# Kernel tuning notes

Hardware: AMD Instinct MI355X
Metric: run time of the kernel (lower is better)

Reference implementation:

```python
import jax, jax.numpy as jnp
import numpy as np

B, C, D = 4096, 1000, 3072


def setup_inputs() -> dict:
    key = jax.random.key(0)
    k1, k2, k3, k4 = jax.random.split(key, 4)
    scale = 1.0
    return {
        "z": jax.random.normal(k1, (B, D), dtype=jnp.float32),
        "sldj": jax.random.normal(k2, (B,), dtype=jnp.float32),
        "labels": jax.random.randint(k3, (B,), 0, C),
        "beta": jnp.ones((), dtype=jnp.float32),
        "means": jax.random.normal(k4, (C, D), dtype=jnp.float32) * scale,
    }


def reference(z, sldj, labels, beta, means):
    # dists[i,j] = -0.5 * ||z_i - mu_j||^2, via a^2 + b^2 - 2ab GEMM trick
    z2 = jnp.sum(z * z, axis=1, keepdims=True)          # [B,1]
    m2 = jnp.sum(means * means, axis=1)[None, :]        # [1,C]
    cross = jnp.einsum('bd,cd->bc', z, means)           # [B,C] GEMM
    dists = -0.5 * (z2 + m2 - 2.0 * cross)              # [B,C]

    log_pz = jax.nn.logsumexp(dists, axis=1)            # [B]
    # cross_entropy(dists, labels) = mean(logsumexp - dists[i, y_i])
    picked = jnp.take_along_axis(dists, labels[:, None], axis=1)[:, 0]
    loss_cls = jnp.mean(log_pz - picked)
    loss_gen = -jnp.mean(log_pz + sldj) / z.shape[1]
    total = loss_gen + beta * loss_cls
    return total, loss_gen, loss_cls
```

## Files before the change

### kernel.cpp

```cpp
#include <hip/hip_runtime.h>
#include <hip/hip_bf16.h>
#include <cstdint>
#include <cstddef>

#define NB 4096
#define NC 1000
#define NCP 1024
#define ND 3072
#define NSL 4
#define KSL (ND / NSL)
#define BM 128
#define BN 128
#define BK 32
#define NT (KSL / BK)
#define ABUF (BM * BK)
#define BBUF (BN * BK)

typedef __attribute__((ext_vector_type(8))) __bf16 bf16x8;
typedef __attribute__((ext_vector_type(4))) float f32x4;
typedef __attribute__((ext_vector_type(4))) unsigned short u16x4;
typedef __attribute__((ext_vector_type(4))) _Float16 f16x4;
typedef unsigned short u16;

__device__ __forceinline__ u16 f2bf_rne(float x) {
    uint32_t u = __float_as_uint(x);
    uint32_t r = (u + 0x7fffu + ((u >> 16) & 1u)) >> 16;
    return (u16)r;
}

__global__ __launch_bounds__(256) void convert_means_kernel(
        const float* __restrict__ means, u16* __restrict__ mb,
        float* __restrict__ m2) {
    const int row = blockIdx.x;
    const int tid = threadIdx.x;
    u16* dst = mb + (size_t)row * ND;
    if (row < NC) {
        const float4* s = (const float4*)(means + (size_t)row * ND);
        float acc = 0.f;
#pragma unroll
        for (int i = 0; i < 3; ++i) {
            const int idx = tid + i * 256;
            float4 v = s[idx];
            acc = fmaf(v.x, v.x, acc);
            acc = fmaf(v.y, v.y, acc);
            acc = fmaf(v.z, v.z, acc);
            acc = fmaf(v.w, v.w, acc);
            u16x4 o;
            o.x = f2bf_rne(v.x); o.y = f2bf_rne(v.y);
            o.z = f2bf_rne(v.z); o.w = f2bf_rne(v.w);
            *(u16x4*)(dst + idx * 4) = o;
        }
#pragma unroll
        for (int off = 32; off > 0; off >>= 1) acc += __shfl_xor(acc, off, 64);
        __shared__ float ssum[4];
        const int wid = tid >> 6, lane = tid & 63;
        if (lane == 0) ssum[wid] = acc;
        __syncthreads();
        if (tid == 0) m2[row] = ssum[0] + ssum[1] + ssum[2] + ssum[3];
    } else {
        u16x4 z4 = (u16x4){0, 0, 0, 0};
#pragma unroll
        for (int i = 0; i < 3; ++i) *(u16x4*)(dst + (tid + i * 256) * 4) = z4;
        if (tid == 0) m2[row] = 1e30f;
    }
}

#define GLOAD_LDS16(gp, lp)                                            \
    __builtin_amdgcn_global_load_lds(                                  \
        (const __attribute__((address_space(1))) void*)(gp),           \
        (__attribute__((address_space(3))) void*)(lp), 16, 0, 0)

__global__ __launch_bounds__(256, 4) void gemm_kernel(
        const float* __restrict__ z, const u16* __restrict__ mb,
        _Float16* __restrict__ crossh, float* __restrict__ z2p) {
    __shared__ u16 As[2 * ABUF];
    __shared__ u16 Bs[2 * BBUF];

    const int tid  = threadIdx.x;
    const int wid  = tid >> 6;
    const int lane = tid & 63;
    const int wr   = wid >> 1;
    const int wc   = wid & 1;
    const int lrow = lane & 15;
    const int kgrp = lane >> 4;

    const int bid = blockIdx.x;
    const int w = (bid & 7) * 128 + (bid >> 3);
    const int bcol8 = w & 7;
    const int brow  = ((w >> 3) & 31) * BM;
    const int ksl   = w >> 8;
    const int bcol  = bcol8 * BN;
    const int kbase = ksl * KSL;
    const bool do_ssq = (bcol8 == 0);

    f32x4 acc[4][4];
#pragma unroll
    for (int m = 0; m < 4; ++m)
#pragma unroll
        for (int n = 0; n < 4; ++n) acc[m][n] = (f32x4){0.f, 0.f, 0.f, 0.f};

    const float* gA[4];
    u16* wAp[4];
#pragma unroll
    for (int g = 0; g < 4; ++g) {
        const int c = g * 256 + tid;
        const int r = c >> 3, q = c & 7;
        const int p = (q >> 1) ^ ((r >> 1) & 3);
        gA[g]  = z + (size_t)(brow + r) * ND + kbase + q * 4;
        wAp[g] = As + r * BK + p * 8 + (q & 1) * 4;
    }
    const u16* gB[2];
    u16* lB[2];
#pragma unroll
    for (int g = 0; g < 2; ++g) {
        const int c = g * 256 + tid;
        const int r = c >> 2, p = c & 3, s = p ^ ((r >> 1) & 3);
        gB[g] = mb + (size_t)(bcol + r) * ND + kbase + s * 8;
        lB[g] = Bs + (g * 256 + wid * 64) * 8;
    }

    float4 areg[4];
    float ssq0 = 0.f, ssq1 = 0.f, ssq2 = 0.f, ssq3 = 0.f;

#define ISSUE(tt, nb_) do {                                              \
        const int ko_ = (tt) * BK;                                       \
        areg[0] = *(const float4*)(gA[0] + ko_);                         \
        areg[1] = *(const float4*)(gA[1] + ko_);                         \
        areg[2] = *(const float4*)(gA[2] + ko_);                         \
        areg[3] = *(const float4*)(gA[3] + ko_);                         \
        GLOAD_LDS16(gB[0] + ko_, lB[0] + (nb_) * BBUF);                  \
        GLOAD_LDS16(gB[1] + ko_, lB[1] + (nb_) * BBUF);                  \
    } while (0)

#define WRITEA(nb_) do {                                                 \
        _Pragma("unroll")                                                \
        for (int g = 0; g < 4; ++g) {                                    \
            u16x4 o;                                                     \
            o.x = f2bf_rne(areg[g].x); o.y = f2bf_rne(areg[g].y);        \
            o.z = f2bf_rne(areg[g].z); o.w = f2bf_rne(areg[g].w);        \
            *(u16x4*)(wAp[g] + (nb_) * ABUF) = o;                        \
        }                                                                \
        if (do_ssq) {                                                    \
            ssq0 = fmaf(areg[0].x, areg[0].x, fmaf(areg[0].y, areg[0].y, \
                   fmaf(areg[0].z, areg[0].z, fmaf(areg[0].w, areg[0].w, ssq0)))); \
            ssq1 = fmaf(areg[1].x, areg[1].x, fmaf(areg[1].y, areg[1].y, \
                   fmaf(areg[1].z, areg[1].z, fmaf(areg[1].w, areg[1].w, ssq1)))); \
            ssq2 = fmaf(areg[2].x, areg[2].x, fmaf(areg[2].y, areg[2].y, \
                   fmaf(areg[2].z, areg[2].z, fmaf(areg[2].w, areg[2].w, ssq2)))); \
            ssq3 = fmaf(areg[3].x, areg[3].x, fmaf(areg[3].y, areg[3].y, \
                   fmaf(areg[3].z, areg[3].z, fmaf(areg[3].w, areg[3].w, ssq3)))); \
        }                                                                \
    } while (0)

#define COMP(tt) do {                                                    \
        const int cb_ = (tt) & 1;                                        \
        const u16* Ac = As + cb_ * ABUF;                                 \
        const u16* Bc = Bs + cb_ * BBUF;                                 \
        const int pk = kgrp ^ ((lrow >> 1) & 3);                         \
        bf16x8 a0 = *(const bf16x8*)&Ac[(wr * 64 +  0 + lrow) * BK + pk * 8]; \
        bf16x8 a1 = *(const bf16x8*)&Ac[(wr * 64 + 16 + lrow) * BK + pk * 8]; \
        bf16x8 a2 = *(const bf16x8*)&Ac[(wr * 64 + 32 + lrow) * BK + pk * 8]; \
        bf16x8 a3 = *(const bf16x8*)&Ac[(wr * 64 + 48 + lrow) * BK + pk * 8]; \
        _Pragma("unroll")                                                \
        for (int n = 0; n < 4; ++n) {                                    \
            bf16x8 bn = *(const bf16x8*)&Bc[(wc * 64 + n * 16 + lrow) * BK + pk * 8]; \
            acc[0][n] = __builtin_amdgcn_mfma_f32_16x16x32_bf16(a0, bn, acc[0][n], 0, 0, 0); \
            acc[1][n] = __builtin_amdgcn_mfma_f32_16x16x32_bf16(a1, bn, acc[1][n], 0, 0, 0); \
            acc[2][n] = __builtin_amdgcn_mfma_f32_16x16x32_bf16(a2, bn, acc[2][n], 0, 0, 0); \
            acc[3][n] = __builtin_amdgcn_mfma_f32_16x16x32_bf16(a3, bn, acc[3][n], 0, 0, 0); \
        }                                                                \
    } while (0)

    ISSUE(0, 0);
    asm volatile("s_waitcnt vmcnt(0)" ::: "memory");
    WRITEA(0);
    asm volatile("s_waitcnt lgkmcnt(0)" ::: "memory");
    __builtin_amdgcn_s_barrier();
    __builtin_amdgcn_sched_barrier(0);

    for (int t = 0; t < NT; ++t) {
        const int nxt = (t + 1) & 1;
        if (t + 1 < NT) ISSUE(t + 1, nxt);
        __builtin_amdgcn_sched_barrier(0);
        COMP(t);
        if (t + 1 < NT) {
            asm volatile("s_waitcnt vmcnt(0)" ::: "memory");
            WRITEA(nxt);
        }
        asm volatile("s_waitcnt lgkmcnt(0)" ::: "memory");
        __builtin_amdgcn_s_barrier();
        __builtin_amdgcn_sched_barrier(0);
    }

#undef ISSUE
#undef WRITEA
#undef COMP

    if (do_ssq) {
        float* sb = (float*)As;
        sb[0 * 256 + tid] = ssq0;
        sb[1 * 256 + tid] = ssq1;
        sb[2 * 256 + tid] = ssq2;
        sb[3 * 256 + tid] = ssq3;
        __syncthreads();
        if (tid < BM) {
            const int g = tid >> 5;
            const int base = (tid * 8) & 255;
            float s = 0.f;
#pragma unroll
            for (int j = 0; j < 8; ++j) s += sb[g * 256 + base + j];
            z2p[(size_t)ksl * NB + brow + tid] = s;
        }
    }

    _Float16* outp = crossh + (size_t)ksl * NB * NCP;
#pragma unroll
    for (int n = 0; n < 4; ++n) {
        const int gcol = bcol + wc * 64 + n * 16 + lrow;
#pragma unroll
        for (int m = 0; m < 4; ++m) {
#pragma unroll
            for (int r = 0; r < 4; ++r) {
                const int grow = brow + wr * 64 + m * 16 + kgrp * 4 + r;
                outp[(size_t)grow * NCP + gcol] = (_Float16)acc[m][n][r];
            }
        }
    }
}

__global__ __launch_bounds__(256) void row_lse_kernel(
        const _Float16* __restrict__ crossh, const float* __restrict__ m2,
        const int* __restrict__ labels, const float* __restrict__ sldj,
        float* __restrict__ outA, float* __restrict__ outB) {
    const int row = blockIdx.x;
    const int tid = threadIdx.x;

    float a0 = 0.f, a1 = 0.f, a2 = 0.f, a3 = 0.f;
#pragma unroll
    for (int s = 0; s < NSL; ++s) {
        f16x4 h = ((const f16x4*)(crossh + ((size_t)s * NB + row) * NCP))[tid];
        a0 += (float)h.x; a1 += (float)h.y; a2 += (float)h.z; a3 += (float)h.w;
    }
    float4 mm = ((const float4*)m2)[tid];
    float4 v;
    v.x = a0 - 0.5f * mm.x;
    v.y = a1 - 0.5f * mm.y;
    v.z = a2 - 0.5f * mm.z;
    v.w = a3 - 0.5f * mm.w;

    float mx = fmaxf(fmaxf(v.x, v.y), fmaxf(v.z, v.w));
#pragma unroll
    for (int off = 32; off > 0; off >>= 1) mx = fmaxf(mx, __shfl_xor(mx, off, 64));
    __shared__ float smax[4], ssum[4];
    const int wid = tid >> 6, lane = tid & 63;
    if (lane == 0) smax[wid] = mx;
    __syncthreads();
    const float bm = fmaxf(fmaxf(smax[0], smax[1]), fmaxf(smax[2], smax[3]));

    float s = expf(v.x - bm) + expf(v.y - bm) + expf(v.z - bm) + expf(v.w - bm);
#pragma unroll
    for (int off = 32; off > 0; off >>= 1) s += __shfl_xor(s, off, 64);
    if (lane == 0) ssum[wid] = s;
    __syncthreads();
    if (tid == 0) {
        const float tot = ssum[0] + ssum[1] + ssum[2] + ssum[3];
        const float lpz = bm + logf(tot);
        const int lab = labels[row];
        float pick = 0.f;
#pragma unroll
        for (int si = 0; si < NSL; ++si)
            pick += (float)crossh[((size_t)si * NB + row) * NCP + lab];
        pick -= 0.5f * m2[lab];
        outA[row] = lpz - pick;
        outB[row] = lpz + sldj[row];
    }
}

__global__ __launch_bounds__(1024) void finalize_kernel(
        const float* __restrict__ a, const float* __restrict__ b,
        const float* __restrict__ z2p, const float* __restrict__ beta,
        float* __restrict__ out) {
    __shared__ float sa[1024], sb[1024], sz[1024];
    const int tid = threadIdx.x;
    float va = 0.f, vb = 0.f, vz = 0.f;
    for (int i = tid; i < NB; i += 1024) { va += a[i]; vb += b[i]; }
    for (int i = tid; i < NSL * NB; i += 1024) vz += z2p[i];
    sa[tid] = va; sb[tid] = vb; sz[tid] = vz;
    __syncthreads();
    for (int s = 512; s > 0; s >>= 1) {
        if (tid < s) {
            sa[tid] += sa[tid + s];
            sb[tid] += sb[tid + s];
            sz[tid] += sz[tid + s];
        }
        __syncthreads();
    }
    if (tid == 0) {
        const float loss_cls = sa[0] / (float)NB;
        const float mean_lpz_sldj = sb[0] / (float)NB - 0.5f * (sz[0] / (float)NB);
        const float loss_gen = -mean_lpz_sldj / (float)ND;
        const float total = loss_gen + beta[0] * loss_cls;
        out[0] = total;
        out[1] = loss_gen;
        out[2] = loss_cls;
    }
}

extern "C" void kernel_launch(void* const* d_in, const int* in_sizes, int n_in,
                              void* d_out, int out_size, void* d_ws, size_t ws_size,
                              hipStream_t stream) {
    const float* z      = (const float*)d_in[0];
    const float* sldj   = (const float*)d_in[1];
    const int*   labels = (const int*)d_in[2];
    const float* beta   = (const float*)d_in[3];
    const float* means  = (const float*)d_in[4];
    float* out = (float*)d_out;

    char* ws = (char*)d_ws;
    size_t off = 0;
    u16* mb = (u16*)(ws + off);           off += (size_t)NCP * ND * 2;
    float* m2 = (float*)(ws + off);       off += (size_t)NCP * 4;
    _Float16* crossh = (_Float16*)(ws + off); off += (size_t)NSL * NB * NCP * 2;
    float* z2p = (float*)(ws + off);      off += (size_t)NSL * NB * 4;
    float* ra = (float*)(ws + off);       off += (size_t)NB * 4;
    float* rb = (float*)(ws + off);       off += (size_t)NB * 4;

    convert_means_kernel<<<NCP, 256, 0, stream>>>(means, mb, m2);
    gemm_kernel<<<8 * 32 * NSL, 256, 0, stream>>>(z, mb, crossh, z2p);
    row_lse_kernel<<<NB, 256, 0, stream>>>(crossh, m2, labels, sldj, ra, rb);
    finalize_kernel<<<1, 1024, 0, stream>>>(ra, rb, z2p, beta, out);
}
```

Measured before the change: 66.99 us.

## Pre-convert z to bf16 in a separate pass and load A tiles directly to LDS

The z matrix is now converted to bf16, and its row squared norms computed, in a combined conversion kernel alongside means. The GEMM then loads both operands with global_load_lds straight into shared memory, so the per-tile register staging, conversion and ssq work disappear from the main loop and the pipeline becomes simpler. The z2 partials per k-slice are replaced by a single z2 vector. The cost is an extra pass over z (reading 50MB of fp32 and writing 25MB of bf16). The GEMM's main loop also now waits on all loads and a barrier before issuing the next stage, which may reduce overlap.

```diff
diff --git a/kernel.cpp b/kernel.cpp
--- a/kernel.cpp
+++ b/kernel.cpp
@@ -28,14 +28,29 @@
     return (u16)r;
 }
 
-__global__ __launch_bounds__(256) void convert_means_kernel(
-        const float* __restrict__ means, u16* __restrict__ mb,
-        float* __restrict__ m2) {
-    const int row = blockIdx.x;
+__global__ __launch_bounds__(256) void convert_all_kernel(
+        const float* __restrict__ z, const float* __restrict__ means,
+        u16* __restrict__ zb, u16* __restrict__ mb,
+        float* __restrict__ z2, float* __restrict__ m2) {
+    const int bidx = blockIdx.x;
     const int tid = threadIdx.x;
-    u16* dst = mb + (size_t)row * ND;
-    if (row < NC) {
-        const float4* s = (const float4*)(means + (size_t)row * ND);
+    const float* src;
+    u16* dst;
+    float* sq;
+    bool pad = false;
+    if (bidx < NB) {
+        src = z + (size_t)bidx * ND;
+        dst = zb + (size_t)bidx * ND;
+        sq = z2 + bidx;
+    } else {
+        const int mr = bidx - NB;
+        dst = mb + (size_t)mr * ND;
+        sq = m2 + mr;
+        src = means + (size_t)mr * ND;
+        pad = (mr >= NC);
+    }
+    if (!pad) {
+        const float4* s = (const float4*)src;
         float acc = 0.f;
 #pragma unroll
         for (int i = 0; i < 3; ++i) {
@@ -56,12 +71,12 @@
         const int wid = tid >> 6, lane = tid & 63;
         if (lane == 0) ssum[wid] = acc;
         __syncthreads();
-        if (tid == 0) m2[row] = ssum[0] + ssum[1] + ssum[2] + ssum[3];
+        if (tid == 0) sq[0] = ssum[0] + ssum[1] + ssum[2] + ssum[3];
     } else {
         u16x4 z4 = (u16x4){0, 0, 0, 0};
 #pragma unroll
         for (int i = 0; i < 3; ++i) *(u16x4*)(dst + (tid + i * 256) * 4) = z4;
-        if (tid == 0) m2[row] = 1e30f;
+        if (tid == 0) sq[0] = 1e30f;
     }
 }
 
@@ -71,8 +86,8 @@
         (__attribute__((address_space(3))) void*)(lp), 16, 0, 0)
 
 __global__ __launch_bounds__(256, 4) void gemm_kernel(
-        const float* __restrict__ z, const u16* __restrict__ mb,
-        _Float16* __restrict__ crossh, float* __restrict__ z2p) {
+        const u16* __restrict__ zb, const u16* __restrict__ mb,
+        _Float16* __restrict__ crossh) {
     __shared__ u16 As[2 * ABUF];
     __shared__ u16 Bs[2 * BBUF];
 
@@ -91,7 +106,6 @@
     const int ksl   = w >> 8;
     const int bcol  = bcol8 * BN;
     const int kbase = ksl * KSL;
-    const bool do_ssq = (bcol8 == 0);
 
     f32x4 acc[4][4];
 #pragma unroll
@@ -99,57 +113,25 @@
 #pragma unroll
         for (int n = 0; n < 4; ++n) acc[m][n] = (f32x4){0.f, 0.f, 0.f, 0.f};
 
-    const float* gA[4];
-    u16* wAp[4];
-#pragma unroll
-    for (int g = 0; g < 4; ++g) {
-        const int c = g * 256 + tid;
-        const int r = c >> 3, q = c & 7;
-        const int p = (q >> 1) ^ ((r >> 1) & 3);
-        gA[g]  = z + (size_t)(brow + r) * ND + kbase + q * 4;
-        wAp[g] = As + r * BK + p * 8 + (q & 1) * 4;
-    }
-    const u16* gB[2];
-    u16* lB[2];
+    const u16* gA[2]; const u16* gB[2];
+    u16* lA[2];       u16* lB[2];
 #pragma unroll
     for (int g = 0; g < 2; ++g) {
         const int c = g * 256 + tid;
         const int r = c >> 2, p = c & 3, s = p ^ ((r >> 1) & 3);
+        gA[g] = zb + (size_t)(brow + r) * ND + kbase + s * 8;
         gB[g] = mb + (size_t)(bcol + r) * ND + kbase + s * 8;
+        lA[g] = As + (g * 256 + wid * 64) * 8;
         lB[g] = Bs + (g * 256 + wid * 64) * 8;
     }
 
-    float4 areg[4];
-    float ssq0 = 0.f, ssq1 = 0.f, ssq2 = 0.f, ssq3 = 0.f;
-
-#define ISSUE(tt, nb_) do {                                              \
+#define STAGE(tt) do {                                                   \
+        const int bb_ = (tt) & 1;                                        \
         const int ko_ = (tt) * BK;                                       \
-        areg[0] = *(const float4*)(gA[0] + ko_);                         \
-        areg[1] = *(const float4*)(gA[1] + ko_);                         \
-        areg[2] = *(const float4*)(gA[2] + ko_);                         \
-        areg[3] = *(const float4*)(gA[3] + ko_);                         \
-        GLOAD_LDS16(gB[0] + ko_, lB[0] + (nb_) * BBUF);                  \
-        GLOAD_LDS16(gB[1] + ko_, lB[1] + (nb_) * BBUF);                  \
-    } while (0)
-
-#define WRITEA(nb_) do {                                                 \
-        _Pragma("unroll")                                                \
-        for (int g = 0; g < 4; ++g) {                                    \
-            u16x4 o;                                                     \
-            o.x = f2bf_rne(areg[g].x); o.y = f2bf_rne(areg[g].y);        \
-            o.z = f2bf_rne(areg[g].z); o.w = f2bf_rne(areg[g].w);        \
-            *(u16x4*)(wAp[g] + (nb_) * ABUF) = o;                        \
-        }                                                                \
-        if (do_ssq) {                                                    \
-            ssq0 = fmaf(areg[0].x, areg[0].x, fmaf(areg[0].y, areg[0].y, \
-                   fmaf(areg[0].z, areg[0].z, fmaf(areg[0].w, areg[0].w, ssq0)))); \
-            ssq1 = fmaf(areg[1].x, areg[1].x, fmaf(areg[1].y, areg[1].y, \
-                   fmaf(areg[1].z, areg[1].z, fmaf(areg[1].w, areg[1].w, ssq1)))); \
-            ssq2 = fmaf(areg[2].x, areg[2].x, fmaf(areg[2].y, areg[2].y, \
-                   fmaf(areg[2].z, areg[2].z, fmaf(areg[2].w, areg[2].w, ssq2)))); \
-            ssq3 = fmaf(areg[3].x, areg[3].x, fmaf(areg[3].y, areg[3].y, \
-                   fmaf(areg[3].z, areg[3].z, fmaf(areg[3].w, areg[3].w, ssq3)))); \
-        }                                                                \
+        GLOAD_LDS16(gA[0] + ko_, lA[0] + bb_ * ABUF);                    \
+        GLOAD_LDS16(gA[1] + ko_, lA[1] + bb_ * ABUF);                    \
+        GLOAD_LDS16(gB[0] + ko_, lB[0] + bb_ * BBUF);                    \
+        GLOAD_LDS16(gB[1] + ko_, lB[1] + bb_ * BBUF);                    \
     } while (0)
 
 #define COMP(tt) do {                                                    \
@@ -171,47 +153,19 @@
         }                                                                \
     } while (0)
 
-    ISSUE(0, 0);
-    asm volatile("s_waitcnt vmcnt(0)" ::: "memory");
-    WRITEA(0);
-    asm volatile("s_waitcnt lgkmcnt(0)" ::: "memory");
-    __builtin_amdgcn_s_barrier();
-    __builtin_amdgcn_sched_barrier(0);
+    STAGE(0);
 
     for (int t = 0; t < NT; ++t) {
-        const int nxt = (t + 1) & 1;
-        if (t + 1 < NT) ISSUE(t + 1, nxt);
+        asm volatile("s_waitcnt vmcnt(0)" ::: "memory");
+        __builtin_amdgcn_s_barrier();
+        __builtin_amdgcn_sched_barrier(0);
+        if (t + 1 < NT) STAGE(t + 1);
         __builtin_amdgcn_sched_barrier(0);
         COMP(t);
-        if (t + 1 < NT) {
-            asm volatile("s_waitcnt vmcnt(0)" ::: "memory");
-            WRITEA(nxt);
-        }
-        asm volatile("s_waitcnt lgkmcnt(0)" ::: "memory");
-        __builtin_amdgcn_s_barrier();
-        __builtin_amdgcn_sched_barrier(0);
-    }
-
-#undef ISSUE
-#undef WRITEA
+    }
+
+#undef STAGE
 #undef COMP
-
-    if (do_ssq) {
-        float* sb = (float*)As;
-        sb[0 * 256 + tid] = ssq0;
-        sb[1 * 256 + tid] = ssq1;
-        sb[2 * 256 + tid] = ssq2;
-        sb[3 * 256 + tid] = ssq3;
-        __syncthreads();
-        if (tid < BM) {
-            const int g = tid >> 5;
-            const int base = (tid * 8) & 255;
-            float s = 0.f;
-#pragma unroll
-            for (int j = 0; j < 8; ++j) s += sb[g * 256 + base + j];
-            z2p[(size_t)ksl * NB + brow + tid] = s;
-        }
-    }
 
     _Float16* outp = crossh + (size_t)ksl * NB * NCP;
 #pragma unroll
@@ -278,13 +232,14 @@
 
 __global__ __launch_bounds__(1024) void finalize_kernel(
         const float* __restrict__ a, const float* __restrict__ b,
-        const float* __restrict__ z2p, const float* __restrict__ beta,
+        const float* __restrict__ z2, const float* __restrict__ beta,
         float* __restrict__ out) {
     __shared__ float sa[1024], sb[1024], sz[1024];
     const int tid = threadIdx.x;
     float va = 0.f, vb = 0.f, vz = 0.f;
-    for (int i = tid; i < NB; i += 1024) { va += a[i]; vb += b[i]; }
-    for (int i = tid; i < NSL * NB; i += 1024) vz += z2p[i];
+    for (int i = tid; i < NB; i += 1024) {
+        va += a[i]; vb += b[i]; vz += z2[i];
+    }
     sa[tid] = va; sb[tid] = vb; sz[tid] = vz;
     __syncthreads();
     for (int s = 512; s > 0; s >>= 1) {
@@ -318,15 +273,16 @@
 
     char* ws = (char*)d_ws;
     size_t off = 0;
+    u16* zb = (u16*)(ws + off);           off += (size_t)NB * ND * 2;
     u16* mb = (u16*)(ws + off);           off += (size_t)NCP * ND * 2;
+    float* z2 = (float*)(ws + off);       off += (size_t)NB * 4;
     float* m2 = (float*)(ws + off);       off += (size_t)NCP * 4;
     _Float16* crossh = (_Float16*)(ws + off); off += (size_t)NSL * NB * NCP * 2;
-    float* z2p = (float*)(ws + off);      off += (size_t)NSL * NB * 4;
     float* ra = (float*)(ws + off);       off += (size_t)NB * 4;
     float* rb = (float*)(ws + off);       off += (size_t)NB * 4;
 
-    convert_means_kernel<<<NCP, 256, 0, stream>>>(means, mb, m2);
-    gemm_kernel<<<8 * 32 * NSL, 256, 0, stream>>>(z, mb, crossh, z2p);
+    convert_all_kernel<<<NB + NCP, 256, 0, stream>>>(z, means, zb, mb, z2, m2);
+    gemm_kernel<<<8 * 32 * NSL, 256, 0, stream>>>(zb, mb, crossh);
     row_lse_kernel<<<NB, 256, 0, stream>>>(crossh, m2, labels, sldj, ra, rb);
-    finalize_kernel<<<1, 1024, 0, stream>>>(ra, rb, z2p, beta, out);
-}
+    finalize_kernel<<<1, 1024, 0, stream>>>(ra, rb, z2, beta, out);
+}
```

Measured after the change: 66.07 us. Within noise of the previous version (-1.4%).
